# Optimization experiments

Hardware: AMD Instinct MI355X
Metric: run time of the kernel (lower is better)

## Reference

```python
import jax, jax.numpy as jnp
import numpy as np
import math

D_MODEL = 1024
BATCH, SEQ = 8, 2048
EPS_ENT = 1e-10
EPS_LN = 1e-5


def setup_inputs() -> dict:
    key = jax.random.key(0)
    kq, kk, kv, kw = jax.random.split(key, 4)
    query = jax.random.normal(kq, (BATCH, SEQ, D_MODEL), dtype=jnp.float32)
    k_ = jax.random.normal(kk, (BATCH, SEQ, D_MODEL), dtype=jnp.float32)
    v_ = jax.random.normal(kv, (BATCH, SEQ, D_MODEL), dtype=jnp.float32)
    harm_w = jax.random.normal(kw, (D_MODEL, D_MODEL), dtype=jnp.float32) / math.sqrt(D_MODEL)
    harm_b = jnp.zeros((D_MODEL,), dtype=jnp.float32)
    norm_gamma = jnp.ones((D_MODEL,), dtype=jnp.float32)
    norm_beta = jnp.zeros((D_MODEL,), dtype=jnp.float32)
    return {"query": query, "key": k_, "value": v_, "harm_w": harm_w,
            "harm_b": harm_b, "norm_gamma": norm_gamma, "norm_beta": norm_beta}


def reference(query, key, value, harm_w, harm_b, norm_gamma, norm_beta):
    scale = jnp.asarray(math.sqrt(D_MODEL), dtype=query.dtype)
    # scores: [B, Sq, Sk]
    scores = jnp.einsum('bqd,bkd->bqk', query, key) / scale
    attention = jax.nn.softmax(scores, axis=-1)
    # dropout p=0 (eval/deterministic)
    # syntony stat (no-grad in original): normalized mean entropy of attention rows
    entropy = -jnp.sum(attention * jnp.log(attention + EPS_ENT), axis=-1)
    max_entropy = math.log(attention.shape[-1])
    syntony = jnp.clip(1.0 - jnp.mean(entropy) / max_entropy, 0.0, 1.0)
    # output: [B, Sq, D]
    output = jnp.einsum('bqk,bkd->bqd', attention, value)
    # harmonize: linear then syntonic norm (layernorm-style) over feature dim
    h = jnp.einsum('bqd,de->bqe', output, harm_w) + harm_b
    mu = jnp.mean(h, axis=-1, keepdims=True)
    var = jnp.var(h, axis=-1, keepdims=True)
    out = (h - mu) * jax.lax.rsqrt(var + EPS_LN) * norm_gamma + norm_beta
    return out, syntony
```

## Files before the change

kernel.cpp:

```cpp
#include <hip/hip_runtime.h>
#include <math.h>

#define D_MODEL 1024
#define SEQ 2048
#define BATCH 8
#define ROWS (BATCH*SEQ)

typedef __attribute__((ext_vector_type(8))) short bf16x8;
typedef __attribute__((ext_vector_type(4))) float f32x4;

__device__ __forceinline__ unsigned short f2bf(float f) {
  union { float f; unsigned u; } x; x.f = f;
  unsigned r = x.u + 0x7fffu + ((x.u >> 16) & 1u);
  return (unsigned short)(r >> 16);
}

__device__ __forceinline__ void gld16(const unsigned short* g, unsigned short* l) {
  __builtin_amdgcn_global_load_lds(
      (const __attribute__((address_space(1))) unsigned int*)g,
      (__attribute__((address_space(3))) unsigned int*)l, 16, 0, 0);
}

#define BAR() __builtin_amdgcn_s_barrier()
#define LDSOFF(p) ((unsigned)(size_t)(__attribute__((address_space(3))) unsigned short*)(p))

template<int EPI>
__global__ __launch_bounds__(512, 2)
void gemm_b(const unsigned short* __restrict__ A, const unsigned short* __restrict__ B,
            void* __restrict__ Cp, int lda, int ldb, int ldc, int K,
            size_t sA, size_t sB, size_t sC, float scale,
            float* __restrict__ lsum, float* __restrict__ tsum, int lstride,
            const float* __restrict__ bias)
{
  __shared__ __align__(16) unsigned short S[2][2][2][8192];
  const int tid  = threadIdx.x;
  const int lane = tid & 63;
  const int wid  = tid >> 6;
  const int quad = lane >> 4, l16 = lane & 15;
  const int wr = wid >> 2, wc = wid & 3;

  int bx = blockIdx.x, by = blockIdx.y, bz = blockIdx.z;
  {
    const int nx = gridDim.x, ny = gridDim.y;
    const int nwg = nx * ny * gridDim.z;
    const int wg  = bx + nx * (by + ny * bz);
    const int cpx = nwg >> 3;
    int idx = (wg & 7) * cpx + (wg >> 3);
    bx = idx % nx; idx /= nx;
    by = idx % ny; bz = idx / ny;
  }
  const int m0 = by * 256, n0 = bx * 256;

  const int sr = tid >> 2;
  const int u  = ((tid & 3) - (sr >> 1)) & 3;
  const unsigned short* Ag0 = A + (size_t)bz * sA + (size_t)(m0 + sr) * lda + u * 8;
  const unsigned short* Ag1 = Ag0 + (size_t)128 * lda;
  const unsigned short* Bg0 = B + (size_t)bz * sB + (size_t)(n0 + sr) * ldb + u * 8;
  const unsigned short* Bg1 = Bg0 + (size_t)128 * ldb;
  const int ldst = tid * 8;

  f32x4 acc[8][4];
#pragma unroll
  for (int i = 0; i < 8; i++)
#pragma unroll
    for (int j = 0; j < 4; j++) acc[i][j] = (f32x4){0.f, 0.f, 0.f, 0.f};

  const int NT = K >> 6;
  bf16x8 af[8], bfr[4];

#define STG(mat, bufp, ks, koff) do { \
    gld16(((mat) ? Bg0 : Ag0) + (koff), &S[bufp][mat][ks][ldst]); \
    gld16(((mat) ? Bg1 : Ag1) + (koff), &S[bufp][mat][ks][4096 + ldst]); \
  } while (0)

#define LOAD_A8(ks, P) do { \
    const int R0 = wr * 128 + l16; \
    const int s = (quad + (R0 >> 1)) & 3; \
    const unsigned offA = LDSOFF(&S[P][0][ks][R0 * 32 + s * 8]); \
    asm volatile("ds_read_b128 %0, %1 offset:0"    : "=v"(af[0]) : "v"(offA)); \
    asm volatile("ds_read_b128 %0, %1 offset:1024" : "=v"(af[1]) : "v"(offA)); \
    asm volatile("ds_read_b128 %0, %1 offset:2048" : "=v"(af[2]) : "v"(offA)); \
    asm volatile("ds_read_b128 %0, %1 offset:3072" : "=v"(af[3]) : "v"(offA)); \
    asm volatile("ds_read_b128 %0, %1 offset:4096" : "=v"(af[4]) : "v"(offA)); \
    asm volatile("ds_read_b128 %0, %1 offset:5120" : "=v"(af[5]) : "v"(offA)); \
    asm volatile("ds_read_b128 %0, %1 offset:6144" : "=v"(af[6]) : "v"(offA)); \
    asm volatile("ds_read_b128 %0, %1 offset:7168" : "=v"(af[7]) : "v"(offA)); \
  } while (0)

#define LOAD_B4(ks, P) do { \
    const int R0 = wc * 64 + l16; \
    const int s = (quad + (R0 >> 1)) & 3; \
    const unsigned offB = LDSOFF(&S[P][1][ks][R0 * 32 + s * 8]); \
    asm volatile("ds_read_b128 %0, %1 offset:0"    : "=v"(bfr[0]) : "v"(offB)); \
    asm volatile("ds_read_b128 %0, %1 offset:1024" : "=v"(bfr[1]) : "v"(offB)); \
    asm volatile("ds_read_b128 %0, %1 offset:2048" : "=v"(bfr[2]) : "v"(offB)); \
    asm volatile("ds_read_b128 %0, %1 offset:3072" : "=v"(bfr[3]) : "v"(offB)); \
  } while (0)

#define MWAIT() do { \
    asm volatile("s_waitcnt lgkmcnt(0)" ::: "memory"); \
    __builtin_amdgcn_sched_barrier(0); \
  } while (0)

#define MFMA32() do { \
    _Pragma("unroll") \
    for (int i = 0; i < 8; i++) \
    _Pragma("unroll") \
    for (int j = 0; j < 4; j++) \
      acc[i][j] = __builtin_amdgcn_mfma_f32_16x16x32_bf16( \
          af[i], bfr[j], acc[i][j], 0, 0, 0); \
  } while (0)

#define TILE_BODY(P, v) do { \
    const int kHi = ((v) + 1) * 64 + 32; \
    const int kLo = ((v) + 2) * 64; \
     \
    LOAD_A8(0, P); LOAD_B4(0, P); \
    if ((v) + 1 < NT) { STG(0, (P) ^ 1, 1, kHi); STG(1, (P) ^ 1, 1, kHi); } \
    BAR(); MWAIT(); \
    __builtin_amdgcn_s_setprio(1); MFMA32(); __builtin_amdgcn_s_setprio(0); \
    BAR(); \
     \
    LOAD_A8(1, P); LOAD_B4(1, P); \
    if ((v) + 2 < NT) { STG(0, P, 0, kLo); STG(1, P, 0, kLo); } \
    BAR(); MWAIT(); \
    __builtin_amdgcn_s_setprio(1); MFMA32(); __builtin_amdgcn_s_setprio(0); \
     \
    if ((v) + 1 < NT) { \
      if ((v) + 2 < NT) asm volatile("s_waitcnt vmcnt(4)" ::: "memory"); \
      else              asm volatile("s_waitcnt vmcnt(0)" ::: "memory"); \
    } \
    BAR(); \
  } while (0)

  STG(0, 0, 0, 0);  STG(1, 0, 0, 0);
  STG(0, 0, 1, 32); STG(1, 0, 1, 32);
  if (NT > 1) { STG(0, 1, 0, 64); STG(1, 1, 0, 64); }

  if (NT > 1) asm volatile("s_waitcnt vmcnt(4)" ::: "memory");
  else        asm volatile("s_waitcnt vmcnt(0)" ::: "memory");
  BAR();

  for (int v = 0; v < NT; v += 2) {
    TILE_BODY(0, v);
    TILE_BODY(1, v + 1);
  }

#undef TILE_BODY
#undef STG
#undef LOAD_A8
#undef LOAD_B4
#undef MWAIT
#undef MFMA32

  if constexpr (EPI == 0) {
    unsigned short* C = (unsigned short*)Cp + (size_t)bz * sC;
#pragma unroll
    for (int mi = 0; mi < 8; mi++)
#pragma unroll
      for (int r = 0; r < 4; r++) {
        const int grow = m0 + wr * 128 + mi * 16 + quad * 4 + r;
#pragma unroll
        for (int ni = 0; ni < 4; ni++) {
          const int gcol = n0 + wc * 64 + ni * 16 + l16;
          C[(size_t)grow * ldc + gcol] = f2bf(acc[mi][ni][r]);
        }
      }
  } else if constexpr (EPI == 1) {
    unsigned short* C = (unsigned short*)Cp + (size_t)bz * sC;
#pragma unroll
    for (int mi = 0; mi < 8; mi++)
#pragma unroll
      for (int r = 0; r < 4; r++) {
        const int grow = m0 + wr * 128 + mi * 16 + quad * 4 + r;
        float es = 0.f, ts = 0.f;
#pragma unroll
        for (int ni = 0; ni < 4; ni++) {
          const int gcol = n0 + wc * 64 + ni * 16 + l16;
          float s = acc[mi][ni][r] * scale;
          float e = __expf(s);
          es += e; ts += s * e;
          C[(size_t)grow * ldc + gcol] = f2bf(e);
        }
#pragma unroll
        for (int off = 1; off < 16; off <<= 1) {
          es += __shfl_xor(es, off, 64);
          ts += __shfl_xor(ts, off, 64);
        }
        if (l16 == 0) {
          atomicAdd(&lsum[bz * lstride + grow], es);
          atomicAdd(&tsum[bz * lstride + grow], ts);
        }
      }
  } else {
    float* C = (float*)Cp + (size_t)bz * sC;
#pragma unroll
    for (int mi = 0; mi < 8; mi++)
#pragma unroll
      for (int r = 0; r < 4; r++) {
        const int grow = m0 + wr * 128 + mi * 16 + quad * 4 + r;
        const float linv = 1.0f / lsum[bz * lstride + grow];
#pragma unroll
        for (int ni = 0; ni < 4; ni++) {
          const int gcol = n0 + wc * 64 + ni * 16 + l16;
          C[(size_t)grow * ldc + gcol] = acc[mi][ni][r] * linv + bias[gcol];
        }
      }
  }
}

__global__ __launch_bounds__(256)
void cvt_k(const float* __restrict__ src, unsigned short* __restrict__ dst, int n8)
{
  int stride = gridDim.x * 256;
  for (int i = blockIdx.x * 256 + threadIdx.x; i < n8; i += stride) {
    const float4* s = (const float4*)(src + (size_t)i * 8);
    float4 a = s[0], b = s[1];
    union { unsigned short v[8]; uint4 u; } o;
    o.v[0] = f2bf(a.x); o.v[1] = f2bf(a.y); o.v[2] = f2bf(a.z); o.v[3] = f2bf(a.w);
    o.v[4] = f2bf(b.x); o.v[5] = f2bf(b.y); o.v[6] = f2bf(b.z); o.v[7] = f2bf(b.w);
    *(uint4*)(dst + (size_t)i * 8) = o.u;
  }
}

__global__ __launch_bounds__(256)
void wtr_k(const float* __restrict__ W, unsigned short* __restrict__ WT)
{
  __shared__ float t[32][33];
  int bx = blockIdx.x * 32, by = blockIdx.y * 32;
  int tx = threadIdx.x & 31, ty = threadIdx.x >> 5;
#pragma unroll
  for (int i = 0; i < 32; i += 8)
    t[ty + i][tx] = W[(size_t)(by + ty + i) * D_MODEL + bx + tx];
  __syncthreads();
#pragma unroll
  for (int i = 0; i < 32; i += 8)
    WT[(size_t)(bx + ty + i) * D_MODEL + by + tx] = f2bf(t[tx][ty + i]);
}

__global__ __launch_bounds__(256)
void ln_k(float* __restrict__ out, const float* __restrict__ gamma,
          const float* __restrict__ beta)
{
  const size_t row = blockIdx.x;
  float4* p = (float4*)(out + row * D_MODEL);
  const int tid = threadIdx.x;
  float4 v = p[tid];
  float s  = v.x + v.y + v.z + v.w;
  float sq = v.x * v.x + v.y * v.y + v.z * v.z + v.w * v.w;
#pragma unroll
  for (int off = 1; off < 64; off <<= 1) {
    s  += __shfl_xor(s, off, 64);
    sq += __shfl_xor(sq, off, 64);
  }
  __shared__ float sh[8];
  int wv = tid >> 6, lane = tid & 63;
  if (lane == 0) { sh[wv] = s; sh[4 + wv] = sq; }
  __syncthreads();
  s  = sh[0] + sh[1] + sh[2] + sh[3];
  sq = sh[4] + sh[5] + sh[6] + sh[7];
  float mean = s * (1.f / 1024.f);
  float var  = sq * (1.f / 1024.f) - mean * mean;
  float rstd = rsqrtf(var + 1e-5f);
  float4 g = ((const float4*)gamma)[tid];
  float4 b = ((const float4*)beta)[tid];
  v.x = (v.x - mean) * rstd * g.x + b.x;
  v.y = (v.y - mean) * rstd * g.y + b.y;
  v.z = (v.z - mean) * rstd * g.z + b.z;
  v.w = (v.w - mean) * rstd * g.w + b.w;
  p[tid] = v;
}

__global__ __launch_bounds__(256)
void syn_k(const float* __restrict__ l, const float* __restrict__ t,
           float* __restrict__ out)
{
  float s = 0.f;
  for (int r = threadIdx.x; r < ROWS; r += 256) {
    float lv = l[r];
    s += logf(lv) - t[r] / lv;
  }
#pragma unroll
  for (int off = 1; off < 64; off <<= 1) s += __shfl_xor(s, off, 64);
  __shared__ float sh[4];
  if ((threadIdx.x & 63) == 0) sh[threadIdx.x >> 6] = s;
  __syncthreads();
  if (threadIdx.x == 0) {
    float tot  = sh[0] + sh[1] + sh[2] + sh[3];
    float ment = tot / (float)ROWS;
    float syn  = 1.0f - ment / logf((float)SEQ);
    syn = fminf(fmaxf(syn, 0.f), 1.f);
    out[(size_t)ROWS * D_MODEL] = syn;
  }
}

extern "C" void kernel_launch(void* const* d_in, const int* in_sizes, int n_in,
                              void* d_out, int out_size, void* d_ws, size_t ws_size,
                              hipStream_t stream)
{
  const float* q     = (const float*)d_in[0];
  const float* k     = (const float*)d_in[1];
  const float* v     = (const float*)d_in[2];
  const float* hw    = (const float*)d_in[3];
  const float* hb    = (const float*)d_in[4];
  const float* gamma = (const float*)d_in[5];
  const float* beta  = (const float*)d_in[6];
  float* out = (float*)d_out;

  const size_t MB = 1024ull * 1024ull;
  char* ws = (char*)d_ws;
  unsigned short* P   = (unsigned short*)(ws);
  unsigned short* VWT = (unsigned short*)(ws + 64 * MB);
  float* lsum = (float*)(ws + 96 * MB);
  float* tsum = lsum + ROWS;

  unsigned short* Vb = (unsigned short*)out;
  unsigned short* WT = (unsigned short*)((char*)out + 32 * MB);
  unsigned short* Qb = (unsigned short*)out;
  unsigned short* Kb = (unsigned short*)((char*)out + 32 * MB);

  hipMemsetAsync(lsum, 0, 2 * ROWS * sizeof(float), stream);

  const int n8 = ROWS * D_MODEL / 8;

  cvt_k<<<4096, 256, 0, stream>>>(v, Vb, n8);
  wtr_k<<<dim3(32, 32), 256, 0, stream>>>(hw, WT);
  gemm_b<0><<<dim3(ROWS / 256, D_MODEL / 256, 1), 512, 0, stream>>>(
      WT, Vb, VWT, D_MODEL, D_MODEL, ROWS, D_MODEL,
      0, 0, 0, 1.f, nullptr, nullptr, 0, nullptr);

  cvt_k<<<4096, 256, 0, stream>>>(q, Qb, n8);
  cvt_k<<<4096, 256, 0, stream>>>(k, Kb, n8);
  gemm_b<1><<<dim3(SEQ / 256, SEQ / 256, BATCH), 512, 0, stream>>>(
      Qb, Kb, P, D_MODEL, D_MODEL, SEQ, D_MODEL,
      (size_t)SEQ * D_MODEL, (size_t)SEQ * D_MODEL, (size_t)SEQ * SEQ,
      0.03125f, lsum, tsum, SEQ, nullptr);

  gemm_b<2><<<dim3(D_MODEL / 256, SEQ / 256, BATCH), 512, 0, stream>>>(
      P, VWT, out, SEQ, ROWS, D_MODEL, SEQ,
      (size_t)SEQ * SEQ, (size_t)SEQ, (size_t)SEQ * D_MODEL,
      1.f, lsum, tsum, SEQ, hb);

  ln_k<<<ROWS, 256, 0, stream>>>(out, gamma, beta);
  syn_k<<<1, 256, 0, stream>>>(lsum, tsum, out);
}
```

Before: 491.9 us.

## Shrink GEMM tile to 128x256 with K=32 steps and raise occupancy

The bf16 MFMA GEMM tile drops from 256x256 to 128x256, and each pipeline stage now covers K=32 instead of two K=32 halves of a K=64 step. LDS use and accumulator registers are halved so launch bounds can request 4 blocks per CU, and the grids double in the M dimension. The aim is more resident waves to hide latency and a simpler one-barrier-pair-per-stage pipeline. The cost is lower arithmetic intensity per tile, more global traffic for the shared B operand, and more frequent barriers.

```diff
diff --git a/kernel.cpp b/kernel.cpp
--- a/kernel.cpp
+++ b/kernel.cpp
@@ -25,14 +25,15 @@
 #define LDSOFF(p) ((unsigned)(size_t)(__attribute__((address_space(3))) unsigned short*)(p))
 
 template<int EPI>
-__global__ __launch_bounds__(512, 2)
+__global__ __launch_bounds__(512, 4)
 void gemm_b(const unsigned short* __restrict__ A, const unsigned short* __restrict__ B,
             void* __restrict__ Cp, int lda, int ldb, int ldc, int K,
             size_t sA, size_t sB, size_t sC, float scale,
             float* __restrict__ lsum, float* __restrict__ tsum, int lstride,
             const float* __restrict__ bias)
 {
-  __shared__ __align__(16) unsigned short S[2][2][2][8192];
+  __shared__ __align__(16) unsigned short SA[2][128 * 32];
+  __shared__ __align__(16) unsigned short SB[2][256 * 32];
   const int tid  = threadIdx.x;
   const int lane = tid & 63;
   const int wid  = tid >> 6;
@@ -49,48 +50,44 @@
     bx = idx % nx; idx /= nx;
     by = idx % ny; bz = idx / ny;
   }
-  const int m0 = by * 256, n0 = bx * 256;
+  const int m0 = by * 128, n0 = bx * 256;
 
   const int sr = tid >> 2;
   const int u  = ((tid & 3) - (sr >> 1)) & 3;
-  const unsigned short* Ag0 = A + (size_t)bz * sA + (size_t)(m0 + sr) * lda + u * 8;
-  const unsigned short* Ag1 = Ag0 + (size_t)128 * lda;
+  const unsigned short* Ag  = A + (size_t)bz * sA + (size_t)(m0 + sr) * lda + u * 8;
   const unsigned short* Bg0 = B + (size_t)bz * sB + (size_t)(n0 + sr) * ldb + u * 8;
   const unsigned short* Bg1 = Bg0 + (size_t)128 * ldb;
   const int ldst = tid * 8;
 
-  f32x4 acc[8][4];
-#pragma unroll
-  for (int i = 0; i < 8; i++)
+  f32x4 acc[4][4];
+#pragma unroll
+  for (int i = 0; i < 4; i++)
 #pragma unroll
     for (int j = 0; j < 4; j++) acc[i][j] = (f32x4){0.f, 0.f, 0.f, 0.f};
 
-  const int NT = K >> 6;
-  bf16x8 af[8], bfr[4];
-
-#define STG(mat, bufp, ks, koff) do { \
-    gld16(((mat) ? Bg0 : Ag0) + (koff), &S[bufp][mat][ks][ldst]); \
-    gld16(((mat) ? Bg1 : Ag1) + (koff), &S[bufp][mat][ks][4096 + ldst]); \
-  } while (0)
-
-#define LOAD_A8(ks, P) do { \
-    const int R0 = wr * 128 + l16; \
+  const int NT = K >> 5;
+  bf16x8 af[4], bfr[4];
+
+#define STG(P, koff) do { \
+    gld16(Ag  + (koff), &SA[P][ldst]); \
+    gld16(Bg0 + (koff), &SB[P][ldst]); \
+    gld16(Bg1 + (koff), &SB[P][4096 + ldst]); \
+  } while (0)
+
+#define LOAD_A4(P) do { \
+    const int R0 = wr * 64 + l16; \
     const int s = (quad + (R0 >> 1)) & 3; \
-    const unsigned offA = LDSOFF(&S[P][0][ks][R0 * 32 + s * 8]); \
+    const unsigned offA = LDSOFF(&SA[P][R0 * 32 + s * 8]); \
     asm volatile("ds_read_b128 %0, %1 offset:0"    : "=v"(af[0]) : "v"(offA)); \
     asm volatile("ds_read_b128 %0, %1 offset:1024" : "=v"(af[1]) : "v"(offA)); \
     asm volatile("ds_read_b128 %0, %1 offset:2048" : "=v"(af[2]) : "v"(offA)); \
     asm volatile("ds_read_b128 %0, %1 offset:3072" : "=v"(af[3]) : "v"(offA)); \
-    asm volatile("ds_read_b128 %0, %1 offset:4096" : "=v"(af[4]) : "v"(offA)); \
-    asm volatile("ds_read_b128 %0, %1 offset:5120" : "=v"(af[5]) : "v"(offA)); \
-    asm volatile("ds_read_b128 %0, %1 offset:6144" : "=v"(af[6]) : "v"(offA)); \
-    asm volatile("ds_read_b128 %0, %1 offset:7168" : "=v"(af[7]) : "v"(offA)); \
-  } while (0)
-
-#define LOAD_B4(ks, P) do { \
+  } while (0)
+
+#define LOAD_B4(P) do { \
     const int R0 = wc * 64 + l16; \
     const int s = (quad + (R0 >> 1)) & 3; \
-    const unsigned offB = LDSOFF(&S[P][1][ks][R0 * 32 + s * 8]); \
+    const unsigned offB = LDSOFF(&SB[P][R0 * 32 + s * 8]); \
     asm volatile("ds_read_b128 %0, %1 offset:0"    : "=v"(bfr[0]) : "v"(offB)); \
     asm volatile("ds_read_b128 %0, %1 offset:1024" : "=v"(bfr[1]) : "v"(offB)); \
     asm volatile("ds_read_b128 %0, %1 offset:2048" : "=v"(bfr[2]) : "v"(offB)); \
@@ -102,9 +99,9 @@
     __builtin_amdgcn_sched_barrier(0); \
   } while (0)
 
-#define MFMA32() do { \
+#define MFMA16() do { \
     _Pragma("unroll") \
-    for (int i = 0; i < 8; i++) \
+    for (int i = 0; i < 4; i++) \
     _Pragma("unroll") \
     for (int j = 0; j < 4; j++) \
       acc[i][j] = __builtin_amdgcn_mfma_f32_16x16x32_bf16( \
@@ -112,33 +109,19 @@
   } while (0)
 
 #define TILE_BODY(P, v) do { \
-    const int kHi = ((v) + 1) * 64 + 32; \
-    const int kLo = ((v) + 2) * 64; \
-     \
-    LOAD_A8(0, P); LOAD_B4(0, P); \
-    if ((v) + 1 < NT) { STG(0, (P) ^ 1, 1, kHi); STG(1, (P) ^ 1, 1, kHi); } \
-    BAR(); MWAIT(); \
-    __builtin_amdgcn_s_setprio(1); MFMA32(); __builtin_amdgcn_s_setprio(0); \
-    BAR(); \
-     \
-    LOAD_A8(1, P); LOAD_B4(1, P); \
-    if ((v) + 2 < NT) { STG(0, P, 0, kLo); STG(1, P, 0, kLo); } \
-    BAR(); MWAIT(); \
-    __builtin_amdgcn_s_setprio(1); MFMA32(); __builtin_amdgcn_s_setprio(0); \
-     \
-    if ((v) + 1 < NT) { \
-      if ((v) + 2 < NT) asm volatile("s_waitcnt vmcnt(4)" ::: "memory"); \
-      else              asm volatile("s_waitcnt vmcnt(0)" ::: "memory"); \
-    } \
-    BAR(); \
-  } while (0)
-
-  STG(0, 0, 0, 0);  STG(1, 0, 0, 0);
-  STG(0, 0, 1, 32); STG(1, 0, 1, 32);
-  if (NT > 1) { STG(0, 1, 0, 64); STG(1, 1, 0, 64); }
-
-  if (NT > 1) asm volatile("s_waitcnt vmcnt(4)" ::: "memory");
-  else        asm volatile("s_waitcnt vmcnt(0)" ::: "memory");
+    LOAD_A4(P); LOAD_B4(P); \
+    MWAIT(); \
+    __builtin_amdgcn_s_setprio(1); MFMA16(); __builtin_amdgcn_s_setprio(0); \
+    BAR();                                     \
+    if ((v) + 2 < NT) STG(P, ((v) + 2) * 32); \
+    if ((v) + 2 < NT)      asm volatile("s_waitcnt vmcnt(3)" ::: "memory"); \
+    else if ((v) + 1 < NT) asm volatile("s_waitcnt vmcnt(0)" ::: "memory"); \
+    BAR();                                     \
+  } while (0)
+
+  STG(0, 0);
+  STG(1, 32);
+  asm volatile("s_waitcnt vmcnt(3)" ::: "memory");
   BAR();
 
   for (int v = 0; v < NT; v += 2) {
@@ -148,18 +131,18 @@
 
 #undef TILE_BODY
 #undef STG
-#undef LOAD_A8
+#undef LOAD_A4
 #undef LOAD_B4
 #undef MWAIT
-#undef MFMA32
+#undef MFMA16
 
   if constexpr (EPI == 0) {
     unsigned short* C = (unsigned short*)Cp + (size_t)bz * sC;
 #pragma unroll
-    for (int mi = 0; mi < 8; mi++)
+    for (int mi = 0; mi < 4; mi++)
 #pragma unroll
       for (int r = 0; r < 4; r++) {
-        const int grow = m0 + wr * 128 + mi * 16 + quad * 4 + r;
+        const int grow = m0 + wr * 64 + mi * 16 + quad * 4 + r;
 #pragma unroll
         for (int ni = 0; ni < 4; ni++) {
           const int gcol = n0 + wc * 64 + ni * 16 + l16;
@@ -169,10 +152,10 @@
   } else if constexpr (EPI == 1) {
     unsigned short* C = (unsigned short*)Cp + (size_t)bz * sC;
 #pragma unroll
-    for (int mi = 0; mi < 8; mi++)
+    for (int mi = 0; mi < 4; mi++)
 #pragma unroll
       for (int r = 0; r < 4; r++) {
-        const int grow = m0 + wr * 128 + mi * 16 + quad * 4 + r;
+        const int grow = m0 + wr * 64 + mi * 16 + quad * 4 + r;
         float es = 0.f, ts = 0.f;
 #pragma unroll
         for (int ni = 0; ni < 4; ni++) {
@@ -195,10 +178,10 @@
   } else {
     float* C = (float*)Cp + (size_t)bz * sC;
 #pragma unroll
-    for (int mi = 0; mi < 8; mi++)
+    for (int mi = 0; mi < 4; mi++)
 #pragma unroll
       for (int r = 0; r < 4; r++) {
-        const int grow = m0 + wr * 128 + mi * 16 + quad * 4 + r;
+        const int grow = m0 + wr * 64 + mi * 16 + quad * 4 + r;
         const float linv = 1.0f / lsum[bz * lstride + grow];
 #pragma unroll
         for (int ni = 0; ni < 4; ni++) {
@@ -325,18 +308,18 @@
 
   cvt_k<<<4096, 256, 0, stream>>>(v, Vb, n8);
   wtr_k<<<dim3(32, 32), 256, 0, stream>>>(hw, WT);
-  gemm_b<0><<<dim3(ROWS / 256, D_MODEL / 256, 1), 512, 0, stream>>>(
+  gemm_b<0><<<dim3(ROWS / 256, D_MODEL / 128, 1), 512, 0, stream>>>(
       WT, Vb, VWT, D_MODEL, D_MODEL, ROWS, D_MODEL,
       0, 0, 0, 1.f, nullptr, nullptr, 0, nullptr);
 
   cvt_k<<<4096, 256, 0, stream>>>(q, Qb, n8);
   cvt_k<<<4096, 256, 0, stream>>>(k, Kb, n8);
-  gemm_b<1><<<dim3(SEQ / 256, SEQ / 256, BATCH), 512, 0, stream>>>(
+  gemm_b<1><<<dim3(SEQ / 256, SEQ / 128, BATCH), 512, 0, stream>>>(
       Qb, Kb, P, D_MODEL, D_MODEL, SEQ, D_MODEL,
       (size_t)SEQ * D_MODEL, (size_t)SEQ * D_MODEL, (size_t)SEQ * SEQ,
       0.03125f, lsum, tsum, SEQ, nullptr);
 
-  gemm_b<2><<<dim3(D_MODEL / 256, SEQ / 256, BATCH), 512, 0, stream>>>(
+  gemm_b<2><<<dim3(D_MODEL / 256, SEQ / 128, BATCH), 512, 0, stream>>>(
       P, VWT, out, SEQ, ROWS, D_MODEL, SEQ,
       (size_t)SEQ * SEQ, (size_t)SEQ, (size_t)SEQ * D_MODEL,
       1.f, lsum, tsum, SEQ, hb);
```

After: 490.1 us. No clear change (-0.4%).
